# Kernel tuning notes

Hardware: AMD Instinct MI355X
Metric: run time of the kernel (lower is better)

The kernel has to match this reference:

```python
import jax, jax.numpy as jnp
import numpy as np

NEG_INF = -9e15  # matches the source's -9000000000000000.0 mask fill
ALPHA = 0.2      # leaky_relu negative slope


def setup_inputs() -> dict:
    key = jax.random.key(0)
    k1, k2, k3, k4 = jax.random.split(key, 4)
    B, N, C_IN, C_OUT, H = 2, 2048, 128, 128, 16
    c = C_OUT // H  # 8 per-head features; equals H//2 so source's a-slice is consistent
    node_feats = jax.random.normal(k1, (B, N, C_IN), dtype=jnp.float32)
    # random 0/1 adjacency with self-loops
    adj = jax.random.randint(k2, (B, N, N), 0, 2).astype(jnp.float32)
    adj = jnp.maximum(adj, jnp.eye(N, dtype=jnp.float32)[None])
    # glorot-uniform-ish params
    W = jax.random.normal(k3, (C_IN, H * c), dtype=jnp.float32) * np.sqrt(2.0 / (C_IN + H * c))
    b = jnp.zeros((H * c,), dtype=jnp.float32)
    a = jax.random.normal(k4, (H, 2 * c), dtype=jnp.float32) * np.sqrt(2.0 / (H + 2 * c))
    return {"node_feats": node_feats, "adj_matrix": adj, "W": W, "b": b, "a": a}


def reference(node_feats, adj_matrix, W, b, a):
    B, N = node_feats.shape[:2]
    H = a.shape[0]
    c = a.shape[1] // 2
    # projection + split into heads: [B, N, H, c]
    h = (node_feats @ W + b).reshape(B, N, H, c)
    # additive attention halves (source slices a along last axis)
    logit_parent = jnp.einsum('bnhc,hc->bnh', h, a[:, :c])
    logit_child = jnp.einsum('bnhc,hc->bnh', h, a[:, c:])
    # dense broadcast-add logits: [B, N(i), N(j), H]
    attn_logits = logit_parent[:, :, None, :] + logit_child[:, None, :, :]
    attn_logits = jax.nn.leaky_relu(attn_logits, negative_slope=ALPHA)
    attn_logits = jnp.where(adj_matrix[..., None] == 1.0, attn_logits, NEG_INF)
    attn_probs = jax.nn.softmax(attn_logits, axis=2)  # over source nodes j
    out = jnp.einsum('bijh,bjhc->bihc', attn_probs, h)
    out = out.reshape(B, N, H * c)  # concat_heads=True
    return out, adj_matrix
```

## Files before the change

### kernel.cpp

```cpp
#include <hip/hip_runtime.h>
#include <hip/hip_bf16.h>


#define B_   2
#define N_   2048
#define CIN_ 128
#define H_   16

typedef _Float16 h2  __attribute__((ext_vector_type(2)));
typedef _Float16 v8h __attribute__((ext_vector_type(8)));
typedef float    v4f __attribute__((ext_vector_type(4)));

#define SC6 0.015625f

__device__ inline h2 pk_f16(float a, float b) {
  return __builtin_bit_cast(h2, __builtin_amdgcn_cvt_pkrtz(a, b));
}
__device__ inline unsigned as_u32(h2 v) { return __builtin_bit_cast(unsigned, v); }
__device__ inline h2 as_h2(unsigned u) { return __builtin_bit_cast(h2, u); }

__global__ __launch_bounds__(128) void proj_kernel(
    const float* __restrict__ nf, const float* __restrict__ W,
    const float* __restrict__ bias, const float* __restrict__ a,
    unsigned* __restrict__ hQ, unsigned* __restrict__ qI,
    float* __restrict__ lpT, unsigned* __restrict__ ones) {
  const int row0 = blockIdx.x * 4;
  const int t    = threadIdx.x;
  if (blockIdx.x == 0) {
    ones[t] = 0x3C003C00u; ones[t + 128] = 0x3C003C00u;
    ones[t + 256] = 0x3C003C00u; ones[t + 384] = 0x3C003C00u;
  }
  __shared__ float sNf[4][CIN_];
  ((float4*)&sNf[0][0])[t] = ((const float4*)(nf + (long)row0 * CIN_))[t];
  __syncthreads();
  float acc[4];
  const float bv = bias[t];
#pragma unroll
  for (int r = 0; r < 4; ++r) acc[r] = bv;
#pragma unroll 8
  for (int k = 0; k < CIN_; ++k) {
    const float w = W[k * 128 + t];
#pragma unroll
    for (int r = 0; r < 4; ++r) acc[r] = fmaf(sNf[r][k], w, acc[r]);
  }
  const int h = t >> 3, kc = t & 7;
  const int b = row0 >> 11, n0 = row0 & (N_ - 1);
  const int bh = b * H_ + h;
  const int cdw = n0 >> 1;
  uint2 hv;
  hv.x = as_u32(pk_f16(acc[0], acc[1]));
  hv.y = as_u32(pk_f16(acc[2], acc[3]));
  *(uint2*)(hQ + ((long)(bh * 8 + kc)) * (N_ / 2) + cdw) = hv;

  const float ap = a[h * 16 + kc], ac = a[h * 16 + 8 + kc];
  float lpv[4], lcv[4];
#pragma unroll
  for (int r = 0; r < 4; ++r) {
    float x = acc[r] * ap, y = acc[r] * ac;
#pragma unroll
    for (int s = 1; s < 8; s <<= 1) {
      x += __shfl_xor(x, s);
      y += __shfl_xor(y, s);
    }
    lpv[r] = x; lcv[r] = y;
  }
  if (kc == 0) {
    float4 l0 = {lpv[0], lpv[1], lpv[2], lpv[3]};
    *(float4*)(lpT + (long)bh * N_ + n0) = l0;
    uint2 q1, q2;
    q1.x = as_u32(pk_f16(__expf(lcv[0]) * SC6, __expf(lcv[1]) * SC6));
    q1.y = as_u32(pk_f16(__expf(lcv[2]) * SC6, __expf(lcv[3]) * SC6));
    q2.x = as_u32(pk_f16(__expf(0.2f * lcv[0]) * SC6, __expf(0.2f * lcv[1]) * SC6));
    q2.y = as_u32(pk_f16(__expf(0.2f * lcv[2]) * SC6, __expf(0.2f * lcv[3]) * SC6));
    const int addr = bh * 2048 + (cdw >> 4) * 32 + ((cdw >> 2) & 3) * 8;
    const int off  = cdw & 3;
    *(uint2*)(qI + addr + off)     = q1;
    *(uint2*)(qI + addr + 4 + off) = q2;
  }
}

__global__ __launch_bounds__(512) void attn_kernel(
    const float* __restrict__ adj, const unsigned* __restrict__ hQ,
    const unsigned* __restrict__ qI, const float* __restrict__ lpT,
    const unsigned* __restrict__ ones, float* __restrict__ pA,
    float* __restrict__ pL, float* __restrict__ adj_out) {
  const int jq     = blockIdx.x & 3;
  const int hgroup = (blockIdx.x >> 2) & 1;
  const int rest   = blockIdx.x >> 3;
  const int b      = rest >> 6;
  const int i0     = (rest & 63) * 32;
  const int tid    = threadIdx.x;
  const int w      = tid >> 6;
  const int lane   = tid & 63;

  __shared__ uint4 sA[2048];

  {
    const long aoff = (long)(b * N_ + i0) * N_ + jq * 512;
    const float* abase = adj + aoff;
    float* obase = adj_out + aoff;
#pragma unroll
    for (int s = 0; s < 4; ++s) {
      const int D = s * 512 + tid;
      const int u = D >> 10, loc = D & 1023;
      const int mm = loc & 15, qc = loc >> 4;
      const int cc = (qc >> 2) * 32 + (qc & 3) * 8;
      const int row = u * 16 + mm;
      const float4 fa = *(const float4*)(abase + (long)row * N_ + cc);
      const float4 fb = *(const float4*)(abase + (long)row * N_ + cc + 4);
      uint4 uu;
      uu.x = as_u32(pk_f16(fa.x, fa.y)); uu.y = as_u32(pk_f16(fa.z, fa.w));
      uu.z = as_u32(pk_f16(fb.x, fb.y)); uu.w = as_u32(pk_f16(fb.z, fb.w));
      sA[D] = uu;
      if (hgroup == 0) {
        *(float4*)(obase + (long)row * N_ + cc)     = fa;
        *(float4*)(obase + (long)row * N_ + cc + 4) = fb;
      }
    }
  }
  __syncthreads();

  const int hw = hgroup * 8 + w;
  const int bh = b * H_ + hw;
  const int m  = lane & 15;
  const int q  = lane >> 4;

  const float lpa = lpT[(long)bh * N_ + i0 + m];
  const float lpb = lpT[(long)bh * N_ + i0 + 16 + m];
  const h2 P1a = pk_f16(__expf(lpa) * SC6, __expf(lpa) * SC6);
  const h2 P2a = pk_f16(__expf(0.2f * lpa) * SC6, __expf(0.2f * lpa) * SC6);
  const h2 P1b = pk_f16(__expf(lpb) * SC6, __expf(lpb) * SC6);
  const h2 P2b = pk_f16(__expf(0.2f * lpb) * SC6, __expf(0.2f * lpb) * SC6);

  const unsigned* qp = qI + bh * 2048 + jq * 512 + q * 8;
  const unsigned* hp = (m < 8)
      ? hQ + ((long)(bh * 8 + m)) * (N_ / 2) + jq * 256 + q * 4
      : ones + q * 4;

  v4f acc0 = {0.0f, 0.0f, 0.0f, 0.0f};
  v4f acc1 = {0.0f, 0.0f, 0.0f, 0.0f};

  uint4 q1A = *(const uint4*)(qp),      q2A = *(const uint4*)(qp + 4),
        hA  = *(const uint4*)(hp);
  uint4 q1B = *(const uint4*)(qp + 32), q2B = *(const uint4*)(qp + 36),
        hB  = *(const uint4*)(hp + 16);

  for (int t2 = 0; t2 < 8; ++t2) {
    const int ch0 = 2 * t2, ch1 = 2 * t2 + 1;
    const int pq0 = ((ch0 + 2) & 15) * 32, ph0 = ((ch0 + 2) & 15) * 16;
    const int pq1 = ((ch1 + 2) & 15) * 32, ph1 = ((ch1 + 2) & 15) * 16;

    const uint4 q1n0 = *(const uint4*)(qp + pq0);
    const uint4 q2n0 = *(const uint4*)(qp + pq0 + 4);
    const uint4 hn0  = *(const uint4*)(hp + ph0);
    {
      const uint4 Av0 = sA[ch0 * 64 + lane];
      const uint4 Av1 = sA[1024 + ch0 * 64 + lane];
      const v8h bf = __builtin_bit_cast(v8h, hA);
      const h2 Q1x = as_h2(q1A.x), Q1y = as_h2(q1A.y), Q1z = as_h2(q1A.z), Q1w = as_h2(q1A.w);
      const h2 Q2x = as_h2(q2A.x), Q2y = as_h2(q2A.y), Q2z = as_h2(q2A.z), Q2w = as_h2(q2A.w);
      const uint4 af0 = {
        as_u32(__builtin_elementwise_max(P1a * Q1x, P2a * Q2x) * as_h2(Av0.x)),
        as_u32(__builtin_elementwise_max(P1a * Q1y, P2a * Q2y) * as_h2(Av0.y)),
        as_u32(__builtin_elementwise_max(P1a * Q1z, P2a * Q2z) * as_h2(Av0.z)),
        as_u32(__builtin_elementwise_max(P1a * Q1w, P2a * Q2w) * as_h2(Av0.w))};
      acc0 = __builtin_amdgcn_mfma_f32_16x16x32_f16(
          __builtin_bit_cast(v8h, af0), bf, acc0, 0, 0, 0);
      const uint4 af1 = {
        as_u32(__builtin_elementwise_max(P1b * Q1x, P2b * Q2x) * as_h2(Av1.x)),
        as_u32(__builtin_elementwise_max(P1b * Q1y, P2b * Q2y) * as_h2(Av1.y)),
        as_u32(__builtin_elementwise_max(P1b * Q1z, P2b * Q2z) * as_h2(Av1.z)),
        as_u32(__builtin_elementwise_max(P1b * Q1w, P2b * Q2w) * as_h2(Av1.w))};
      acc1 = __builtin_amdgcn_mfma_f32_16x16x32_f16(
          __builtin_bit_cast(v8h, af1), bf, acc1, 0, 0, 0);
    }
    q1A = q1n0; q2A = q2n0; hA = hn0;

    const uint4 q1n1 = *(const uint4*)(qp + pq1);
    const uint4 q2n1 = *(const uint4*)(qp + pq1 + 4);
    const uint4 hn1  = *(const uint4*)(hp + ph1);
    {
      const uint4 Av0 = sA[ch1 * 64 + lane];
      const uint4 Av1 = sA[1024 + ch1 * 64 + lane];
      const v8h bf = __builtin_bit_cast(v8h, hB);
      const h2 Q1x = as_h2(q1B.x), Q1y = as_h2(q1B.y), Q1z = as_h2(q1B.z), Q1w = as_h2(q1B.w);
      const h2 Q2x = as_h2(q2B.x), Q2y = as_h2(q2B.y), Q2z = as_h2(q2B.z), Q2w = as_h2(q2B.w);
      const uint4 af0 = {
        as_u32(__builtin_elementwise_max(P1a * Q1x, P2a * Q2x) * as_h2(Av0.x)),
        as_u32(__builtin_elementwise_max(P1a * Q1y, P2a * Q2y) * as_h2(Av0.y)),
        as_u32(__builtin_elementwise_max(P1a * Q1z, P2a * Q2z) * as_h2(Av0.z)),
        as_u32(__builtin_elementwise_max(P1a * Q1w, P2a * Q2w) * as_h2(Av0.w))};
      acc0 = __builtin_amdgcn_mfma_f32_16x16x32_f16(
          __builtin_bit_cast(v8h, af0), bf, acc0, 0, 0, 0);
      const uint4 af1 = {
        as_u32(__builtin_elementwise_max(P1b * Q1x, P2b * Q2x) * as_h2(Av1.x)),
        as_u32(__builtin_elementwise_max(P1b * Q1y, P2b * Q2y) * as_h2(Av1.y)),
        as_u32(__builtin_elementwise_max(P1b * Q1z, P2b * Q2z) * as_h2(Av1.z)),
        as_u32(__builtin_elementwise_max(P1b * Q1w, P2b * Q2w) * as_h2(Av1.w))};
      acc1 = __builtin_amdgcn_mfma_f32_16x16x32_f16(
          __builtin_bit_cast(v8h, af1), bf, acc1, 0, 0, 0);
    }
    q1B = q1n1; q2B = q2n1; hB = hn1;
  }

#pragma unroll
  for (int u = 0; u < 2; ++u) {
    const v4f av = u ? acc1 : acc0;
#pragma unroll
    for (int r = 0; r < 4; ++r) {
      const int gidx = (b * N_ + i0 + u * 16 + q * 4 + r) * H_ + hw;
      if (m < 8)  pA[jq * 524288 + (long)gidx * 8 + m] = av[r];
      if (m == 8) pL[jq * 65536 + gidx] = av[r];
    }
  }
}

__global__ __launch_bounds__(512) void combine_kernel(
    const float* __restrict__ pA, const float* __restrict__ pL,
    float* __restrict__ out) {
  const int g = blockIdx.x * 512 + threadIdx.x;
  const int gl = g >> 3;
  const float s = pL[gl] + pL[gl + 65536] + pL[gl + 131072] + pL[gl + 196608];
  const float v = pA[g] + pA[g + 524288] + pA[g + 1048576] + pA[g + 1572864];
  out[g] = v / s;
}

extern "C" void kernel_launch(void* const* d_in, const int* in_sizes, int n_in,
                              void* d_out, int out_size, void* d_ws, size_t ws_size,
                              hipStream_t stream) {
  const float* nf   = (const float*)d_in[0];
  const float* adj  = (const float*)d_in[1];
  const float* W    = (const float*)d_in[2];
  const float* bias = (const float*)d_in[3];
  const float* a    = (const float*)d_in[4];

  float* out     = (float*)d_out;
  float* adj_out = out + (long)B_ * N_ * H_ * 8;

  unsigned* ws   = (unsigned*)d_ws;
  unsigned* hQ   = ws;
  unsigned* qI   = ws + 262144;
  float*    lpT  = (float*)(ws + 327680);
  unsigned* ones = ws + 393216;
  float*    pA   = (float*)(ws + 393728);
  float*    pL   = (float*)(ws + 2490880);

  hipLaunchKernelGGL(proj_kernel, dim3(B_ * N_ / 4), dim3(128), 0, stream,
                     nf, W, bias, a, hQ, qI, lpT, ones);
  hipLaunchKernelGGL(attn_kernel, dim3(B_ * (N_ / 32) * 2 * 4), dim3(512), 0,
                     stream, adj, hQ, qI, lpT, ones, pA, pL, adj_out);
  hipLaunchKernelGGL(combine_kernel, dim3(1024), dim3(512), 0, stream,
                     pA, pL, out);
}
```

Before: 131.4 us.

## Process all 16 heads per block to read each adjacency tile once

Before, each adjacency tile was loaded and converted to fp16 by two blocks, one per head group. Now a single block does it, and each wave computes two heads, one from each group. This halves the global adjacency reads and the LDS staging work. The adj loads are also all issued before the convert/store phase to increase memory-level parallelism. In exchange the grid shrinks to 512 blocks and registers per thread grow (double accumulators and prefetch buffers), which may cut occupancy and latency hiding.

```diff
diff --git a/kernel.cpp b/kernel.cpp
--- a/kernel.cpp
+++ b/kernel.cpp
@@ -84,14 +84,13 @@
     const unsigned* __restrict__ qI, const float* __restrict__ lpT,
     const unsigned* __restrict__ ones, float* __restrict__ pA,
     float* __restrict__ pL, float* __restrict__ adj_out) {
-  const int jq     = blockIdx.x & 3;
-  const int hgroup = (blockIdx.x >> 2) & 1;
-  const int rest   = blockIdx.x >> 3;
-  const int b      = rest >> 6;
-  const int i0     = (rest & 63) * 32;
-  const int tid    = threadIdx.x;
-  const int w      = tid >> 6;
-  const int lane   = tid & 63;
+  const int jq   = blockIdx.x & 3;
+  const int rest = blockIdx.x >> 2;
+  const int b    = rest >> 6;
+  const int i0   = (rest & 63) * 32;
+  const int tid  = threadIdx.x;
+  const int w    = tid >> 6;
+  const int lane = tid & 63;
 
   __shared__ uint4 sA[2048];
 
@@ -99,118 +98,190 @@
     const long aoff = (long)(b * N_ + i0) * N_ + jq * 512;
     const float* abase = adj + aoff;
     float* obase = adj_out + aoff;
+    float4 fa[4], fb[4];
+    int rowv[4], ccv[4];
 #pragma unroll
     for (int s = 0; s < 4; ++s) {
       const int D = s * 512 + tid;
       const int u = D >> 10, loc = D & 1023;
       const int mm = loc & 15, qc = loc >> 4;
-      const int cc = (qc >> 2) * 32 + (qc & 3) * 8;
-      const int row = u * 16 + mm;
-      const float4 fa = *(const float4*)(abase + (long)row * N_ + cc);
-      const float4 fb = *(const float4*)(abase + (long)row * N_ + cc + 4);
+      ccv[s] = (qc >> 2) * 32 + (qc & 3) * 8;
+      rowv[s] = u * 16 + mm;
+      fa[s] = *(const float4*)(abase + (long)rowv[s] * N_ + ccv[s]);
+      fb[s] = *(const float4*)(abase + (long)rowv[s] * N_ + ccv[s] + 4);
+    }
+#pragma unroll
+    for (int s = 0; s < 4; ++s) {
+      const int D = s * 512 + tid;
       uint4 uu;
-      uu.x = as_u32(pk_f16(fa.x, fa.y)); uu.y = as_u32(pk_f16(fa.z, fa.w));
-      uu.z = as_u32(pk_f16(fb.x, fb.y)); uu.w = as_u32(pk_f16(fb.z, fb.w));
+      uu.x = as_u32(pk_f16(fa[s].x, fa[s].y)); uu.y = as_u32(pk_f16(fa[s].z, fa[s].w));
+      uu.z = as_u32(pk_f16(fb[s].x, fb[s].y)); uu.w = as_u32(pk_f16(fb[s].z, fb[s].w));
       sA[D] = uu;
-      if (hgroup == 0) {
-        *(float4*)(obase + (long)row * N_ + cc)     = fa;
-        *(float4*)(obase + (long)row * N_ + cc + 4) = fb;
-      }
+      *(float4*)(obase + (long)rowv[s] * N_ + ccv[s])     = fa[s];
+      *(float4*)(obase + (long)rowv[s] * N_ + ccv[s] + 4) = fb[s];
     }
   }
   __syncthreads();
 
-  const int hw = hgroup * 8 + w;
-  const int bh = b * H_ + hw;
   const int m  = lane & 15;
   const int q  = lane >> 4;
-
-  const float lpa = lpT[(long)bh * N_ + i0 + m];
-  const float lpb = lpT[(long)bh * N_ + i0 + 16 + m];
-  const h2 P1a = pk_f16(__expf(lpa) * SC6, __expf(lpa) * SC6);
-  const h2 P2a = pk_f16(__expf(0.2f * lpa) * SC6, __expf(0.2f * lpa) * SC6);
-  const h2 P1b = pk_f16(__expf(lpb) * SC6, __expf(lpb) * SC6);
-  const h2 P2b = pk_f16(__expf(0.2f * lpb) * SC6, __expf(0.2f * lpb) * SC6);
-
-  const unsigned* qp = qI + bh * 2048 + jq * 512 + q * 8;
-  const unsigned* hp = (m < 8)
-      ? hQ + ((long)(bh * 8 + m)) * (N_ / 2) + jq * 256 + q * 4
+  const int bh0 = b * H_ + w;
+  const int bh1 = bh0 + 8;
+
+  const float lpa0 = lpT[(long)bh0 * N_ + i0 + m];
+  const float lpb0 = lpT[(long)bh0 * N_ + i0 + 16 + m];
+  const float lpa1 = lpT[(long)bh1 * N_ + i0 + m];
+  const float lpb1 = lpT[(long)bh1 * N_ + i0 + 16 + m];
+  const h2 P1a0 = pk_f16(__expf(lpa0) * SC6, __expf(lpa0) * SC6);
+  const h2 P2a0 = pk_f16(__expf(0.2f * lpa0) * SC6, __expf(0.2f * lpa0) * SC6);
+  const h2 P1b0 = pk_f16(__expf(lpb0) * SC6, __expf(lpb0) * SC6);
+  const h2 P2b0 = pk_f16(__expf(0.2f * lpb0) * SC6, __expf(0.2f * lpb0) * SC6);
+  const h2 P1a1 = pk_f16(__expf(lpa1) * SC6, __expf(lpa1) * SC6);
+  const h2 P2a1 = pk_f16(__expf(0.2f * lpa1) * SC6, __expf(0.2f * lpa1) * SC6);
+  const h2 P1b1 = pk_f16(__expf(lpb1) * SC6, __expf(lpb1) * SC6);
+  const h2 P2b1 = pk_f16(__expf(0.2f * lpb1) * SC6, __expf(0.2f * lpb1) * SC6);
+
+  const unsigned* qp0 = qI + bh0 * 2048 + jq * 512 + q * 8;
+  const unsigned* qp1 = qI + bh1 * 2048 + jq * 512 + q * 8;
+  const unsigned* hp0 = (m < 8)
+      ? hQ + ((long)(bh0 * 8 + m)) * (N_ / 2) + jq * 256 + q * 4
       : ones + q * 4;
-
-  v4f acc0 = {0.0f, 0.0f, 0.0f, 0.0f};
-  v4f acc1 = {0.0f, 0.0f, 0.0f, 0.0f};
-
-  uint4 q1A = *(const uint4*)(qp),      q2A = *(const uint4*)(qp + 4),
-        hA  = *(const uint4*)(hp);
-  uint4 q1B = *(const uint4*)(qp + 32), q2B = *(const uint4*)(qp + 36),
-        hB  = *(const uint4*)(hp + 16);
+  const unsigned* hp1 = (m < 8)
+      ? hQ + ((long)(bh1 * 8 + m)) * (N_ / 2) + jq * 256 + q * 4
+      : ones + q * 4;
+
+  v4f acc0a = {0.f, 0.f, 0.f, 0.f}, acc1a = {0.f, 0.f, 0.f, 0.f};
+  v4f acc0b = {0.f, 0.f, 0.f, 0.f}, acc1b = {0.f, 0.f, 0.f, 0.f};
+
+  uint4 q1X0 = *(const uint4*)(qp0),      q2X0 = *(const uint4*)(qp0 + 4),
+        hX0  = *(const uint4*)(hp0);
+  uint4 q1X1 = *(const uint4*)(qp1),      q2X1 = *(const uint4*)(qp1 + 4),
+        hX1  = *(const uint4*)(hp1);
+  uint4 q1Y0 = *(const uint4*)(qp0 + 32), q2Y0 = *(const uint4*)(qp0 + 36),
+        hY0  = *(const uint4*)(hp0 + 16);
+  uint4 q1Y1 = *(const uint4*)(qp1 + 32), q2Y1 = *(const uint4*)(qp1 + 36),
+        hY1  = *(const uint4*)(hp1 + 16);
 
   for (int t2 = 0; t2 < 8; ++t2) {
     const int ch0 = 2 * t2, ch1 = 2 * t2 + 1;
     const int pq0 = ((ch0 + 2) & 15) * 32, ph0 = ((ch0 + 2) & 15) * 16;
     const int pq1 = ((ch1 + 2) & 15) * 32, ph1 = ((ch1 + 2) & 15) * 16;
 
-    const uint4 q1n0 = *(const uint4*)(qp + pq0);
-    const uint4 q2n0 = *(const uint4*)(qp + pq0 + 4);
-    const uint4 hn0  = *(const uint4*)(hp + ph0);
+    const uint4 n10 = *(const uint4*)(qp0 + pq0);
+    const uint4 n20 = *(const uint4*)(qp0 + pq0 + 4);
+    const uint4 nh0 = *(const uint4*)(hp0 + ph0);
+    const uint4 n11 = *(const uint4*)(qp1 + pq0);
+    const uint4 n21 = *(const uint4*)(qp1 + pq0 + 4);
+    const uint4 nh1 = *(const uint4*)(hp1 + ph0);
     {
       const uint4 Av0 = sA[ch0 * 64 + lane];
       const uint4 Av1 = sA[1024 + ch0 * 64 + lane];
-      const v8h bf = __builtin_bit_cast(v8h, hA);
-      const h2 Q1x = as_h2(q1A.x), Q1y = as_h2(q1A.y), Q1z = as_h2(q1A.z), Q1w = as_h2(q1A.w);
-      const h2 Q2x = as_h2(q2A.x), Q2y = as_h2(q2A.y), Q2z = as_h2(q2A.z), Q2w = as_h2(q2A.w);
-      const uint4 af0 = {
-        as_u32(__builtin_elementwise_max(P1a * Q1x, P2a * Q2x) * as_h2(Av0.x)),
-        as_u32(__builtin_elementwise_max(P1a * Q1y, P2a * Q2y) * as_h2(Av0.y)),
-        as_u32(__builtin_elementwise_max(P1a * Q1z, P2a * Q2z) * as_h2(Av0.z)),
-        as_u32(__builtin_elementwise_max(P1a * Q1w, P2a * Q2w) * as_h2(Av0.w))};
-      acc0 = __builtin_amdgcn_mfma_f32_16x16x32_f16(
-          __builtin_bit_cast(v8h, af0), bf, acc0, 0, 0, 0);
-      const uint4 af1 = {
-        as_u32(__builtin_elementwise_max(P1b * Q1x, P2b * Q2x) * as_h2(Av1.x)),
-        as_u32(__builtin_elementwise_max(P1b * Q1y, P2b * Q2y) * as_h2(Av1.y)),
-        as_u32(__builtin_elementwise_max(P1b * Q1z, P2b * Q2z) * as_h2(Av1.z)),
-        as_u32(__builtin_elementwise_max(P1b * Q1w, P2b * Q2w) * as_h2(Av1.w))};
-      acc1 = __builtin_amdgcn_mfma_f32_16x16x32_f16(
-          __builtin_bit_cast(v8h, af1), bf, acc1, 0, 0, 0);
-    }
-    q1A = q1n0; q2A = q2n0; hA = hn0;
-
-    const uint4 q1n1 = *(const uint4*)(qp + pq1);
-    const uint4 q2n1 = *(const uint4*)(qp + pq1 + 4);
-    const uint4 hn1  = *(const uint4*)(hp + ph1);
+      {
+        const h2 Q1x = as_h2(q1X0.x), Q1y = as_h2(q1X0.y), Q1z = as_h2(q1X0.z), Q1w = as_h2(q1X0.w);
+        const h2 Q2x = as_h2(q2X0.x), Q2y = as_h2(q2X0.y), Q2z = as_h2(q2X0.z), Q2w = as_h2(q2X0.w);
+        const v8h bf = __builtin_bit_cast(v8h, hX0);
+        const uint4 af0 = {
+          as_u32(__builtin_elementwise_max(P1a0 * Q1x, P2a0 * Q2x) * as_h2(Av0.x)),
+          as_u32(__builtin_elementwise_max(P1a0 * Q1y, P2a0 * Q2y) * as_h2(Av0.y)),
+          as_u32(__builtin_elementwise_max(P1a0 * Q1z, P2a0 * Q2z) * as_h2(Av0.z)),
+          as_u32(__builtin_elementwise_max(P1a0 * Q1w, P2a0 * Q2w) * as_h2(Av0.w))};
+        acc0a = __builtin_amdgcn_mfma_f32_16x16x32_f16(
+            __builtin_bit_cast(v8h, af0), bf, acc0a, 0, 0, 0);
+        const uint4 af1 = {
+          as_u32(__builtin_elementwise_max(P1b0 * Q1x, P2b0 * Q2x) * as_h2(Av1.x)),
+          as_u32(__builtin_elementwise_max(P1b0 * Q1y, P2b0 * Q2y) * as_h2(Av1.y)),
+          as_u32(__builtin_elementwise_max(P1b0 * Q1z, P2b0 * Q2z) * as_h2(Av1.z)),
+          as_u32(__builtin_elementwise_max(P1b0 * Q1w, P2b0 * Q2w) * as_h2(Av1.w))};
+        acc1a = __builtin_amdgcn_mfma_f32_16x16x32_f16(
+            __builtin_bit_cast(v8h, af1), bf, acc1a, 0, 0, 0);
+      }
+      {
+        const h2 Q1x = as_h2(q1X1.x), Q1y = as_h2(q1X1.y), Q1z = as_h2(q1X1.z), Q1w = as_h2(q1X1.w);
+        const h2 Q2x = as_h2(q2X1.x), Q2y = as_h2(q2X1.y), Q2z = as_h2(q2X1.z), Q2w = as_h2(q2X1.w);
+        const v8h bf = __builtin_bit_cast(v8h, hX1);
+        const uint4 af0 = {
+          as_u32(__builtin_elementwise_max(P1a1 * Q1x, P2a1 * Q2x) * as_h2(Av0.x)),
+          as_u32(__builtin_elementwise_max(P1a1 * Q1y, P2a1 * Q2y) * as_h2(Av0.y)),
+          as_u32(__builtin_elementwise_max(P1a1 * Q1z, P2a1 * Q2z) * as_h2(Av0.z)),
+          as_u32(__builtin_elementwise_max(P1a1 * Q1w, P2a1 * Q2w) * as_h2(Av0.w))};
+        acc0b = __builtin_amdgcn_mfma_f32_16x16x32_f16(
+            __builtin_bit_cast(v8h, af0), bf, acc0b, 0, 0, 0);
+        const uint4 af1 = {
+          as_u32(__builtin_elementwise_max(P1b1 * Q1x, P2b1 * Q2x) * as_h2(Av1.x)),
+          as_u32(__builtin_elementwise_max(P1b1 * Q1y, P2b1 * Q2y) * as_h2(Av1.y)),
+          as_u32(__builtin_elementwise_max(P1b1 * Q1z, P2b1 * Q2z) * as_h2(Av1.z)),
+          as_u32(__builtin_elementwise_max(P1b1 * Q1w, P2b1 * Q2w) * as_h2(Av1.w))};
+        acc1b = __builtin_amdgcn_mfma_f32_16x16x32_f16(
+            __builtin_bit_cast(v8h, af1), bf, acc1b, 0, 0, 0);
+      }
+    }
+    q1X0 = n10; q2X0 = n20; hX0 = nh0;
+    q1X1 = n11; q2X1 = n21; hX1 = nh1;
+
+    const uint4 m10 = *(const uint4*)(qp0 + pq1);
+    const uint4 m20 = *(const uint4*)(qp0 + pq1 + 4);
+    const uint4 mh0 = *(const uint4*)(hp0 + ph1);
+    const uint4 m11 = *(const uint4*)(qp1 + pq1);
+    const uint4 m21 = *(const uint4*)(qp1 + pq1 + 4);
+    const uint4 mh1 = *(const uint4*)(hp1 + ph1);
     {
       const uint4 Av0 = sA[ch1 * 64 + lane];
       const uint4 Av1 = sA[1024 + ch1 * 64 + lane];
-      const v8h bf = __builtin_bit_cast(v8h, hB);
-      const h2 Q1x = as_h2(q1B.x), Q1y = as_h2(q1B.y), Q1z = as_h2(q1B.z), Q1w = as_h2(q1B.w);
-      const h2 Q2x = as_h2(q2B.x), Q2y = as_h2(q2B.y), Q2z = as_h2(q2B.z), Q2w = as_h2(q2B.w);
-      const uint4 af0 = {
-        as_u32(__builtin_elementwise_max(P1a * Q1x, P2a * Q2x) * as_h2(Av0.x)),
-        as_u32(__builtin_elementwise_max(P1a * Q1y, P2a * Q2y) * as_h2(Av0.y)),
-        as_u32(__builtin_elementwise_max(P1a * Q1z, P2a * Q2z) * as_h2(Av0.z)),
-        as_u32(__builtin_elementwise_max(P1a * Q1w, P2a * Q2w) * as_h2(Av0.w))};
-      acc0 = __builtin_amdgcn_mfma_f32_16x16x32_f16(
-          __builtin_bit_cast(v8h, af0), bf, acc0, 0, 0, 0);
-      const uint4 af1 = {
-        as_u32(__builtin_elementwise_max(P1b * Q1x, P2b * Q2x) * as_h2(Av1.x)),
-        as_u32(__builtin_elementwise_max(P1b * Q1y, P2b * Q2y) * as_h2(Av1.y)),
-        as_u32(__builtin_elementwise_max(P1b * Q1z, P2b * Q2z) * as_h2(Av1.z)),
-        as_u32(__builtin_elementwise_max(P1b * Q1w, P2b * Q2w) * as_h2(Av1.w))};
-      acc1 = __builtin_amdgcn_mfma_f32_16x16x32_f16(
-          __builtin_bit_cast(v8h, af1), bf, acc1, 0, 0, 0);
-    }
-    q1B = q1n1; q2B = q2n1; hB = hn1;
-  }
-
-#pragma unroll
-  for (int u = 0; u < 2; ++u) {
-    const v4f av = u ? acc1 : acc0;
-#pragma unroll
-    for (int r = 0; r < 4; ++r) {
-      const int gidx = (b * N_ + i0 + u * 16 + q * 4 + r) * H_ + hw;
-      if (m < 8)  pA[jq * 524288 + (long)gidx * 8 + m] = av[r];
-      if (m == 8) pL[jq * 65536 + gidx] = av[r];
+      {
+        const h2 Q1x = as_h2(q1Y0.x), Q1y = as_h2(q1Y0.y), Q1z = as_h2(q1Y0.z), Q1w = as_h2(q1Y0.w);
+        const h2 Q2x = as_h2(q2Y0.x), Q2y = as_h2(q2Y0.y), Q2z = as_h2(q2Y0.z), Q2w = as_h2(q2Y0.w);
+        const v8h bf = __builtin_bit_cast(v8h, hY0);
+        const uint4 af0 = {
+          as_u32(__builtin_elementwise_max(P1a0 * Q1x, P2a0 * Q2x) * as_h2(Av0.x)),
+          as_u32(__builtin_elementwise_max(P1a0 * Q1y, P2a0 * Q2y) * as_h2(Av0.y)),
+          as_u32(__builtin_elementwise_max(P1a0 * Q1z, P2a0 * Q2z) * as_h2(Av0.z)),
+          as_u32(__builtin_elementwise_max(P1a0 * Q1w, P2a0 * Q2w) * as_h2(Av0.w))};
+        acc0a = __builtin_amdgcn_mfma_f32_16x16x32_f16(
+            __builtin_bit_cast(v8h, af0), bf, acc0a, 0, 0, 0);
+        const uint4 af1 = {
+          as_u32(__builtin_elementwise_max(P1b0 * Q1x, P2b0 * Q2x) * as_h2(Av1.x)),
+          as_u32(__builtin_elementwise_max(P1b0 * Q1y, P2b0 * Q2y) * as_h2(Av1.y)),
+          as_u32(__builtin_elementwise_max(P1b0 * Q1z, P2b0 * Q2z) * as_h2(Av1.z)),
+          as_u32(__builtin_elementwise_max(P1b0 * Q1w, P2b0 * Q2w) * as_h2(Av1.w))};
+        acc1a = __builtin_amdgcn_mfma_f32_16x16x32_f16(
+            __builtin_bit_cast(v8h, af1), bf, acc1a, 0, 0, 0);
+      }
+      {
+        const h2 Q1x = as_h2(q1Y1.x), Q1y = as_h2(q1Y1.y), Q1z = as_h2(q1Y1.z), Q1w = as_h2(q1Y1.w);
+        const h2 Q2x = as_h2(q2Y1.x), Q2y = as_h2(q2Y1.y), Q2z = as_h2(q2Y1.z), Q2w = as_h2(q2Y1.w);
+        const v8h bf = __builtin_bit_cast(v8h, hY1);
+        const uint4 af0 = {
+          as_u32(__builtin_elementwise_max(P1a1 * Q1x, P2a1 * Q2x) * as_h2(Av0.x)),
+          as_u32(__builtin_elementwise_max(P1a1 * Q1y, P2a1 * Q2y) * as_h2(Av0.y)),
+          as_u32(__builtin_elementwise_max(P1a1 * Q1z, P2a1 * Q2z) * as_h2(Av0.z)),
+          as_u32(__builtin_elementwise_max(P1a1 * Q1w, P2a1 * Q2w) * as_h2(Av0.w))};
+        acc0b = __builtin_amdgcn_mfma_f32_16x16x32_f16(
+            __builtin_bit_cast(v8h, af0), bf, acc0b, 0, 0, 0);
+        const uint4 af1 = {
+          as_u32(__builtin_elementwise_max(P1b1 * Q1x, P2b1 * Q2x) * as_h2(Av1.x)),
+          as_u32(__builtin_elementwise_max(P1b1 * Q1y, P2b1 * Q2y) * as_h2(Av1.y)),
+          as_u32(__builtin_elementwise_max(P1b1 * Q1z, P2b1 * Q2z) * as_h2(Av1.z)),
+          as_u32(__builtin_elementwise_max(P1b1 * Q1w, P2b1 * Q2w) * as_h2(Av1.w))};
+        acc1b = __builtin_amdgcn_mfma_f32_16x16x32_f16(
+            __builtin_bit_cast(v8h, af1), bf, acc1b, 0, 0, 0);
+      }
+    }
+    q1Y0 = m10; q2Y0 = m20; hY0 = mh0;
+    q1Y1 = m11; q2Y1 = m21; hY1 = mh1;
+  }
+
+#pragma unroll
+  for (int g = 0; g < 2; ++g) {
+    const int hw = g * 8 + w;
+#pragma unroll
+    for (int u = 0; u < 2; ++u) {
+      const v4f av = g ? (u ? acc1b : acc0b) : (u ? acc1a : acc0a);
+#pragma unroll
+      for (int r = 0; r < 4; ++r) {
+        const int gidx = (b * N_ + i0 + u * 16 + q * 4 + r) * H_ + hw;
+        if (m < 8)  pA[jq * 524288 + (long)gidx * 8 + m] = av[r];
+        if (m == 8) pL[jq * 65536 + gidx] = av[r];
+      }
     }
   }
 }
@@ -247,7 +318,7 @@
 
   hipLaunchKernelGGL(proj_kernel, dim3(B_ * N_ / 4), dim3(128), 0, stream,
                      nf, W, bias, a, hQ, qI, lpT, ones);
-  hipLaunchKernelGGL(attn_kernel, dim3(B_ * (N_ / 32) * 2 * 4), dim3(512), 0,
+  hipLaunchKernelGGL(attn_kernel, dim3(B_ * (N_ / 32) * 4), dim3(512), 0,
                      stream, adj, hQ, qI, lpT, ones, pA, pL, adj_out);
   hipLaunchKernelGGL(combine_kernel, dim3(1024), dim3(512), 0, stream,
                      pA, pL, out);
```

New measurement: 131.1 us. Within noise of the previous version (-0.2%).
